# Kernel optimization log

Hardware: AMD Instinct MI355X
Metric: run time of the kernel (lower is better)

## Reference

```python
import jax, jax.numpy as jnp
import numpy as np

DIM = 1024
N_HEAD = 16
SEQ = 2048
GATE_IN = 12
ROPE_BASE = 10000.0
ATTN_SCALE = 0.1
EPS = 1e-6


def setup_inputs() -> dict:
    key = jax.random.key(0)
    ks = jax.random.split(key, 8)
    std = 0.5 * DIM ** -0.5
    bound = (3.0 ** 0.5) * std
    x = jax.random.normal(ks[0], (1, SEQ, DIM), dtype=jnp.float32)
    v1 = jax.random.normal(ks[1], (1, SEQ, DIM), dtype=jnp.float32)
    Wq = jax.random.uniform(ks[2], (DIM, DIM), jnp.float32, -bound, bound)
    Wk = jax.random.uniform(ks[3], (DIM, DIM), jnp.float32, -bound, bound)
    Wv = jax.random.uniform(ks[4], (DIM, DIM), jnp.float32, -bound, bound)
    # original zero-inits c_proj/attn_gate; use small random so output is non-trivial
    Wproj = jax.random.normal(ks[5], (DIM, DIM), dtype=jnp.float32) * 0.02
    Wgate = jax.random.normal(ks[6], (N_HEAD, GATE_IN), dtype=jnp.float32) * 0.02
    lamb = jnp.float32(0.5)
    return {"x": x, "v1": v1, "Wq": Wq, "Wk": Wk, "Wv": Wv,
            "Wproj": Wproj, "lamb": lamb, "Wgate": Wgate}


def _rms_norm(t):
    return t * jax.lax.rsqrt(jnp.mean(jnp.square(t), axis=-1, keepdims=True) + EPS)


def _rotary(t):
    # t: [B, T, H, hd]; rotates halves per the module's sign convention
    B, T, H, hd = t.shape
    d = hd // 2
    inv_freq = 1.0 / (ROPE_BASE ** (jnp.arange(0, hd, 2, dtype=jnp.float32) / hd))  # [d]
    freqs = jnp.arange(T, dtype=jnp.float32)[:, None] * inv_freq[None, :]  # [T, d]
    cos = jnp.cos(freqs)[None, :, None, :]
    sin = jnp.sin(freqs)[None, :, None, :]
    x1, x2 = t[..., :d], t[..., d:]
    y1 = x1 * cos + x2 * sin
    y2 = -x1 * sin + x2 * cos
    return jnp.concatenate([y1, y2], axis=-1)


def reference(x, v1, Wq, Wk, Wv, Wproj, lamb, Wgate):
    B, T, dim = x.shape
    H = Wgate.shape[0]
    hd = dim // H

    q = (x @ Wq.T).reshape(B, T, H, hd)
    k = (x @ Wk.T).reshape(B, T, H, hd)
    v = (x @ Wv.T).reshape(B, T, H, hd)

    # lambda-blended value mixing with residual value stream v1
    v = (1.0 - lamb) * v + lamb * v1.reshape(B, T, H, hd)

    q, k = _rms_norm(q), _rms_norm(k)
    q, k = _rotary(q), _rotary(k)

    # causal attention with fixed scale 0.1 (flex_attention block-sparse causal)
    scores = jnp.einsum("bthd,bshd->bhts", q, k) * ATTN_SCALE  # [B,H,T,T]
    causal = jnp.tril(jnp.ones((T, T), dtype=bool))
    scores = jnp.where(causal[None, None], scores, jnp.float32(-1e30))
    probs = jax.nn.softmax(scores, axis=-1)
    y = jnp.einsum("bhts,bshd->bthd", probs, v)  # [B,T,H,hd]

    # sigmoid gate from the first 12 channels of x, per head
    gate = jax.nn.sigmoid(x[..., :Wgate.shape[1]] @ Wgate.T)[..., None]  # [B,T,H,1]
    y = (y * gate).reshape(B, T, dim)
    y = y @ Wproj.T
    return y, v1
```

## Files before the change

kernel.cpp:

```cpp
#include <hip/hip_runtime.h>
#include <hip/hip_bf16.h>

#define T_SEQ 2048
#define NH 16
#define HD 64
#define SCALE_LOG2E 0.14426950408889634f

typedef __attribute__((ext_vector_type(8))) short bf16x8;
typedef __attribute__((ext_vector_type(4))) short bf16x4;
typedef __attribute__((ext_vector_type(4))) float f32x4;

__device__ __forceinline__ short f2bs(float f) {
  union { float f; unsigned u; } v; v.f = f;
  unsigned r = v.u + 0x7fffu + ((v.u >> 16) & 1u);
  return (short)(r >> 16);
}

__device__ __forceinline__ float bs2f(short s) {
  union { unsigned u; float f; } v;
  v.u = ((unsigned)(unsigned short)s) << 16;
  return v.f;
}

__device__ __forceinline__ unsigned cvt_pk_bf16(float lo, float hi) {
  unsigned r;
  asm("v_cvt_pk_bf16_f32 %0, %1, %2" : "=v"(r) : "v"(lo), "v"(hi));
  return r;
}

__device__ __forceinline__ void gload16(const short* g, short* l) {
  __builtin_amdgcn_global_load_lds(
      (const __attribute__((address_space(1))) void*)g,
      (__attribute__((address_space(3))) void*)l, 16, 0, 0);
}

__global__ __launch_bounds__(256) void cvtT(const float* __restrict__ x,
                                            const float* __restrict__ wq,
                                            const float* __restrict__ wk,
                                            const float* __restrict__ wv,
                                            const float* __restrict__ wp,
                                            short* __restrict__ xbT,
                                            short* __restrict__ wqkvT,
                                            short* __restrict__ wpjT) {
  __shared__ __attribute__((aligned(16))) short lv[64][136];
  const int rt = blockIdx.x;
  const int tid = threadIdx.x;
  const float* src; short* dst; int srow0, drow0, R;
  if (rt < 32)      { src = x;  dst = xbT;   R = 2048; srow0 = rt * 64;        drow0 = srow0; }
  else if (rt < 48) { src = wq; dst = wqkvT; R = 3072; srow0 = (rt - 32) * 64; drow0 = srow0; }
  else if (rt < 64) { src = wk; dst = wqkvT; R = 3072; srow0 = (rt - 48) * 64; drow0 = srow0 + 1024; }
  else if (rt < 80) { src = wv; dst = wqkvT; R = 3072; srow0 = (rt - 64) * 64; drow0 = srow0 + 2048; }
  else              { src = wp; dst = wpjT;  R = 1024; srow0 = (rt - 80) * 64; drow0 = srow0; }
  const int c0 = blockIdx.y * 16;
  #pragma unroll
  for (int it = 0; it < 8; ++it) {
    int e = it * 256 + tid;
    int r = e >> 5, c4 = e & 31;
    float4 v = *(const float4*)&src[(size_t)(srow0 + r) * 1024 + blockIdx.y * 128 + c4 * 4];
    bf16x4 o; o[0] = f2bs(v.x); o[1] = f2bs(v.y); o[2] = f2bs(v.z); o[3] = f2bs(v.w);
    *(bf16x4*)&lv[r][c4 * 4] = o;
  }
  __syncthreads();
  #pragma unroll
  for (int it = 0; it < 4; ++it) {
    int e = it * 256 + tid;
    int kc = e >> 6, r = e & 63;
    bf16x8 w = *(const bf16x8*)&lv[r][kc * 8];
    *(bf16x8*)&dst[((size_t)(c0 + kc) * R + drow0 + r) * 8] = w;
  }
}

__global__ __launch_bounds__(256) void gate_rope(const float* __restrict__ x,
                                                 const float* __restrict__ Wg,
                                                 float* __restrict__ gate,
                                                 float2* __restrict__ rope) {
  int id = blockIdx.x * 256 + threadIdx.x;
  int t = id >> 4, h = id & 15;
  float acc = 0.f;
  #pragma unroll
  for (int i = 0; i < 12; ++i) acc += x[(size_t)t * 1024 + i] * Wg[h * 12 + i];
  gate[id] = 1.f / (1.f + __expf(-acc));
  #pragma unroll
  for (int j = 0; j < 2; ++j) {
    int e = id * 2 + j;
    int tt = e >> 5, p = e & 31;
    float invf = __builtin_exp2f(-0.41524101186092f * (float)p);
    float s, c;
    sincosf((float)tt * invf, &s, &c);
    rope[e] = make_float2(c, s);
  }
}

struct GemmSmem {
  union {
    struct { short As[3][4][128][8]; short Bs[3][4][128][8]; } g;
    short lv[128][130];
  };
};
template <bool QKV>
__global__ __launch_bounds__(256) void gemm128(const short* __restrict__ A,
                                               const short* __restrict__ B,
                                               float* __restrict__ C,
                                               short* __restrict__ qb,
                                               short* __restrict__ kb,
                                               short* __restrict__ vt,
                                               const float* __restrict__ v1,
                                               const float* __restrict__ lambp,
                                               const float2* __restrict__ rope,
                                               int M, int N, int K) {
  __shared__ GemmSmem sm;
  const int tid = threadIdx.x;
  const int lane = tid & 63, wid = tid >> 6;
  const int lr = lane & 15, lg = lane >> 4;
  const int wm = (wid >> 1) * 64, wn = (wid & 1) * 64;
  const int bm = blockIdx.x * 128, bn = blockIdx.y * 128;
  const short* Ap = A + ((size_t)wid * M + bm + lane) * 8;
  const short* Bp = B + ((size_t)wid * N + bn + lane) * 8;
  f32x4 acc[4][4] = {};
  auto stage = [&](int buf, int k0) {
    gload16(Ap + (size_t)k0 * M,       &sm.g.As[buf][wid][0][0]);
    gload16(Ap + (size_t)k0 * M + 512, &sm.g.As[buf][wid][64][0]);
    gload16(Bp + (size_t)k0 * N,       &sm.g.Bs[buf][wid][0][0]);
    gload16(Bp + (size_t)k0 * N + 512, &sm.g.Bs[buf][wid][64][0]);
  };
  auto compute = [&](int buf) {
    bf16x8 af[4], bfr[4];
    #pragma unroll
    for (int m = 0; m < 4; ++m) af[m] = *(const bf16x8*)&sm.g.As[buf][lg][wm + m * 16 + lr][0];
    #pragma unroll
    for (int n = 0; n < 4; ++n) bfr[n] = *(const bf16x8*)&sm.g.Bs[buf][lg][wn + n * 16 + lr][0];
    #pragma unroll
    for (int m = 0; m < 4; ++m)
      #pragma unroll
      for (int n = 0; n < 4; ++n)
        acc[m][n] = __builtin_amdgcn_mfma_f32_16x16x32_bf16(af[m], bfr[n], acc[m][n], 0, 0, 0);
  };
  const int nsteps = K >> 5;
  stage(0, 0);
  stage(1, 32);
  int cur = 0;
  for (int ks = 0; ks < nsteps - 1; ++ks) {
    asm volatile("s_waitcnt vmcnt(4)" ::: "memory");
    __builtin_amdgcn_s_barrier();
    __builtin_amdgcn_sched_barrier(0);
    int s2 = cur + 2; if (s2 >= 3) s2 -= 3;
    if (ks + 2 < nsteps) stage(s2, (ks + 2) * 32);
    compute(cur);
    cur = (cur == 2) ? 0 : cur + 1;
  }
  asm volatile("s_waitcnt vmcnt(0)" ::: "memory");
  __builtin_amdgcn_s_barrier();
  __builtin_amdgcn_sched_barrier(0);
  compute(cur);

  if constexpr (QKV) {
    if (bn < 2048) {
      const bool isq = (bn < 1024);
      short* dst = isq ? qb : kb;
      const int h = ((bn + wn) & 1023) >> 6;
      #pragma unroll
      for (int m = 0; m < 4; ++m)
        #pragma unroll
        for (int r = 0; r < 4; ++r) {
          const int t = bm + wm + m * 16 + 4 * lg + r;
          float ss = acc[m][0][r] * acc[m][0][r] + acc[m][1][r] * acc[m][1][r]
                   + acc[m][2][r] * acc[m][2][r] + acc[m][3][r] * acc[m][3][r];
          ss += __shfl_xor(ss, 1);
          ss += __shfl_xor(ss, 2);
          ss += __shfl_xor(ss, 4);
          ss += __shfl_xor(ss, 8);
          const float rms = rsqrtf(ss * (1.f / 64.f) + 1e-6f);
          short* row = dst + ((size_t)h * T_SEQ + t) * 64;
          #pragma unroll
          for (int n2 = 0; n2 < 2; ++n2) {
            float x1 = acc[m][n2][r] * rms, x2 = acc[m][n2 + 2][r] * rms;
            float2 cs = rope[t * 32 + n2 * 16 + lr];
            float y1 = x1 * cs.x + x2 * cs.y;
            float y2 = x2 * cs.x - x1 * cs.y;
            if (isq) { y1 *= SCALE_LOG2E; y2 *= SCALE_LOG2E; }
            row[n2 * 16 + lr] = f2bs(y1);
            row[32 + n2 * 16 + lr] = f2bs(y2);
          }
        }
    } else {
      const float Lb = *lambp;
      const int h0 = (bn - 2048) >> 6;
      __syncthreads();
      #pragma unroll
      for (int m = 0; m < 4; ++m)
        #pragma unroll
        for (int r = 0; r < 4; ++r) {
          const int tl = wm + m * 16 + 4 * lg + r;
          const size_t vrow = (size_t)(bm + tl) * 1024 + h0 * 64;
          #pragma unroll
          for (int n = 0; n < 4; ++n) {
            const int col = wn + n * 16 + lr;
            float w = v1[vrow + col];
            sm.lv[tl][col] = f2bs((1.f - Lb) * acc[m][n][r] + Lb * w);
          }
        }
      __syncthreads();
      #pragma unroll
      for (int it = 0; it < 8; ++it) {
        int u = it * 256 + tid;
        int c0 = (u & 15) * 8;
        int d = (u >> 4) & 63;
        int hh = u >> 10;
        bf16x8 w;
        #pragma unroll
        for (int j = 0; j < 8; ++j) {
          int c = c0 + j;
          int src = (c & 96) | ((c & 1) << 4) | ((c >> 1) & 15);
          w[j] = sm.lv[src][hh * 64 + d];
        }
        *(bf16x8*)&vt[((size_t)(h0 + hh) * 64 + d) * T_SEQ + bm + c0] = w;
      }
    }
  } else {
    #pragma unroll
    for (int m = 0; m < 4; ++m)
      #pragma unroll
      for (int r = 0; r < 4; ++r) {
        const int t = bm + wm + m * 16 + 4 * lg + r;
        float* Cr = C + (size_t)t * N + bn + wn + lr;
        #pragma unroll
        for (int n = 0; n < 4; ++n) Cr[n * 16] = acc[m][n][r];
      }
  }
}

__global__ __launch_bounds__(256) void attn(const short* __restrict__ qb,
                                            const short* __restrict__ kb,
                                            const short* __restrict__ vtp,
                                            short* __restrict__ partO,
                                            float* __restrict__ partL) {
  __shared__ __attribute__((aligned(16))) short Ks[2][4096];
  __shared__ __attribute__((aligned(16))) short Vs[2][4096];
  __shared__ __attribute__((aligned(16))) short p_lds[4][16][72];
  const int head = blockIdx.x & 15;
  const int b = blockIdx.x >> 4;
  int strip, qg;
  if (b < 32)      { strip = 0; qg = 31 - b; }
  else if (b < 56) { strip = 1; qg = 63 - b; }
  else if (b < 72) { strip = 2; qg = 87 - b; }
  else             { strip = 3; qg = 103 - b; }
  const int nt = min(8, qg + 1 - strip * 8);
  const int lane = threadIdx.x & 63, wid = threadIdx.x >> 6;
  const int lr = lane & 15, lg = lane >> 4;
  const int qt0 = qg * 64 + wid * 16;
  const short* Q = qb + (size_t)head * (T_SEQ * HD);
  const short* Kp = kb + (size_t)head * (T_SEQ * HD);
  const short* Vt = vtp + (size_t)head * (HD * T_SEQ);
  short (*P)[72] = p_lds[wid];

  bf16x8 aq0 = *(const bf16x8*)&Q[(size_t)(qt0 + lr) * HD + 8 * lg];
  bf16x8 aq1 = *(const bf16x8*)&Q[(size_t)(qt0 + lr) * HD + 32 + 8 * lg];
  f32x4 accO[4] = {};
  float lsum[4] = {0.f, 0.f, 0.f, 0.f};

  auto stage = [&](int buf, int jg) {
    const int kv0 = jg * 64;
    #pragma unroll
    for (int i = 0; i < 2; ++i) {
      int s = i * 256 + wid * 64 + lane;
      int row = s >> 3;
      int cG = (s & 7) ^ (row & 7);
      gload16(Kp + (size_t)(kv0 + row) * HD + cG * 8,
              &Ks[buf][(size_t)(i * 256 + wid * 64) * 8]);
      gload16(Vt + (size_t)row * T_SEQ + kv0 + cG * 8,
              &Vs[buf][(size_t)(i * 256 + wid * 64) * 8]);
    }
  };
  stage(0, strip * 8);
  for (int j = 0; j < nt; ++j) {
    const int jg = strip * 8 + j;
    __syncthreads();
    if (j + 1 < nt) stage((j + 1) & 1, jg + 1);
    const short* Kb = Ks[j & 1];
    const short* Vb = Vs[j & 1];
    f32x4 st[4];
    #pragma unroll
    for (int t = 0; t < 4; ++t) {
      int row = 16 * t + lr;
      int c0 = lg ^ (row & 7);
      bf16x8 k0 = *(const bf16x8*)&Kb[row * 64 + c0 * 8];
      bf16x8 k1 = *(const bf16x8*)&Kb[row * 64 + (c0 ^ 4) * 8];
      f32x4 s = {};
      s = __builtin_amdgcn_mfma_f32_16x16x32_bf16(aq0, k0, s, 0, 0, 0);
      s = __builtin_amdgcn_mfma_f32_16x16x32_bf16(aq1, k1, s, 0, 0, 0);
      st[t] = s;
    }
    if (jg == qg) {
      #pragma unroll
      for (int t = 0; t < 4; ++t)
        #pragma unroll
        for (int r = 0; r < 4; ++r)
          st[t][r] = (16 * t + lr > wid * 16 + 4 * lg + r) ? -1e30f : st[t][r];
    }
    #pragma unroll
    for (int r = 0; r < 4; ++r) {
      float p0 = __builtin_exp2f(st[0][r]);
      float p1 = __builtin_exp2f(st[1][r]);
      float p2 = __builtin_exp2f(st[2][r]);
      float p3 = __builtin_exp2f(st[3][r]);
      lsum[r] += (p0 + p1) + (p2 + p3);
      *(unsigned*)&P[4 * lg + r][2 * lr] = cvt_pk_bf16(p0, p1);
      *(unsigned*)&P[4 * lg + r][32 + 2 * lr] = cvt_pk_bf16(p2, p3);
    }
    asm volatile("s_waitcnt lgkmcnt(0)" ::: "memory");
    __builtin_amdgcn_sched_barrier(0);
    bf16x8 pa0 = *(const bf16x8*)&P[lr][8 * lg];
    bf16x8 pa1 = *(const bf16x8*)&P[lr][32 + 8 * lg];
    #pragma unroll
    for (int nv = 0; nv < 4; ++nv) {
      int row0 = nv * 16 + lr;
      int c0 = lg ^ (row0 & 7);
      bf16x8 v0 = *(const bf16x8*)&Vb[row0 * 64 + c0 * 8];
      bf16x8 v1e = *(const bf16x8*)&Vb[row0 * 64 + (c0 ^ 4) * 8];
      accO[nv] = __builtin_amdgcn_mfma_f32_16x16x32_bf16(pa0, v0, accO[nv], 0, 0, 0);
      accO[nv] = __builtin_amdgcn_mfma_f32_16x16x32_bf16(pa1, v1e, accO[nv], 0, 0, 0);
    }
  }
  short* pO = partO + (size_t)(head * 80 + b) * 4096;
  float* pL = partL + (size_t)(head * 80 + b) * 64;
  #pragma unroll
  for (int r = 0; r < 4; ++r) {
    float sres = lsum[r];
    sres += __shfl_xor(sres, 1);
    sres += __shfl_xor(sres, 2);
    sres += __shfl_xor(sres, 4);
    sres += __shfl_xor(sres, 8);
    int row = wid * 16 + 4 * lg + r;
    #pragma unroll
    for (int nv = 0; nv < 4; ++nv)
      pO[row * 64 + nv * 16 + lr] = f2bs(accO[nv][r]);
    if (lr == 0) pL[row] = sres;
  }
}

__global__ __launch_bounds__(256) void attn_reduce(const short* __restrict__ partO,
                                                   const float* __restrict__ partL,
                                                   const float* __restrict__ gate,
                                                   short* __restrict__ obT) {
  const int head = blockIdx.x & 15;
  const int qg = blockIdx.x >> 4;
  const int ns = (qg >> 3) + 1;
  const int tid = threadIdx.x;
  const int row = tid >> 2, q4 = tid & 3;
  const int sbase[4] = {0, 32, 56, 72};
  f32x4 o[4] = {};
  float l = 0.f;
  for (int s = 0; s < ns; ++s) {
    const int slot = head * 80 + sbase[s] + 31 - qg;
    const short* pb = partO + (size_t)slot * 4096;
    #pragma unroll
    for (int c = 0; c < 4; ++c) {
      bf16x4 v = *(const bf16x4*)&pb[row * 64 + q4 * 16 + c * 4];
      #pragma unroll
      for (int j = 0; j < 4; ++j) o[c][j] += bs2f(v[j]);
    }
    l += partL[(size_t)slot * 64 + row];
  }
  const int t = qg * 64 + row;
  const float gs = gate[t * 16 + head] / l;
  const int cg0 = head * 8 + q4 * 2;
  bf16x8 w0, w1;
  #pragma unroll
  for (int j = 0; j < 4; ++j) {
    w0[j]     = f2bs(o[0][j] * gs);
    w0[4 + j] = f2bs(o[1][j] * gs);
    w1[j]     = f2bs(o[2][j] * gs);
    w1[4 + j] = f2bs(o[3][j] * gs);
  }
  *(bf16x8*)&obT[((size_t)cg0 * 2048 + t) * 8] = w0;
  *(bf16x8*)&obT[((size_t)(cg0 + 1) * 2048 + t) * 8] = w1;
}

extern "C" void kernel_launch(void* const* d_in, const int* in_sizes, int n_in,
                              void* d_out, int out_size, void* d_ws, size_t ws_size,
                              hipStream_t stream) {
  const float* x     = (const float*)d_in[0];
  const float* v1    = (const float*)d_in[1];
  const float* Wq    = (const float*)d_in[2];
  const float* Wk    = (const float*)d_in[3];
  const float* Wv    = (const float*)d_in[4];
  const float* Wproj = (const float*)d_in[5];
  const float* lamb  = (const float*)d_in[6];
  const float* Wgate = (const float*)d_in[7];
  float* out = (float*)d_out;

  char* ws = (char*)d_ws;
  short*  xbT   = (short*)(ws);
  short*  wqkvT = (short*)(ws + ((size_t)4  << 20));
  short*  wpjT  = (short*)(ws + ((size_t)10 << 20));
  short*  partO = (short*)(ws + ((size_t)12 << 20));
  float*  partL = (float*)(ws + ((size_t)23 << 20));
  float2* rope  = (float2*)(ws + ((size_t)34 << 20));
  short*  qb    = (short*)(ws + ((size_t)36 << 20));
  short*  kb    = (short*)(ws + ((size_t)40 << 20));
  short*  vt    = (short*)(ws + ((size_t)44 << 20));
  float*  gate  = (float*)(ws + ((size_t)48 << 20));
  short*  obT   = xbT;

  cvtT<<<dim3(96, 8), 256, 0, stream>>>(x, Wq, Wk, Wv, Wproj, xbT, wqkvT, wpjT);
  gate_rope<<<(T_SEQ * NH) / 256, 256, 0, stream>>>(x, Wgate, gate, rope);
  gemm128<true><<<dim3(16, 24), 256, 0, stream>>>(xbT, wqkvT, nullptr, qb, kb, vt,
                                                  v1, lamb, rope, 2048, 3072, 1024);
  attn<<<1280, 256, 0, stream>>>(qb, kb, vt, partO, partL);
  attn_reduce<<<512, 256, 0, stream>>>(partO, partL, gate, obT);
  gemm128<false><<<dim3(16, 8), 256, 0, stream>>>(obT, wpjT, out, nullptr, nullptr,
                                                  nullptr, nullptr, nullptr, nullptr,
                                                  2048, 1024, 1024);
  hipMemcpyAsync(out + (size_t)T_SEQ * 1024, v1,
                 (size_t)T_SEQ * 1024 * sizeof(float),
                 hipMemcpyDeviceToDevice, stream);
}
```

Measured before the change: 79.89 us.

## Fuse prep kernels, drop split-KV attention reduce, and retile projection GEMM

Merges the conversion, gate/rope computation and the v1 output copy into one prep launch. Attention no longer splits the key range into strips, so it no longer writes partial outputs for a separate reduce kernel. Each block now walks the full causal range and applies the normalization and gate directly. The output projection GEMM uses 64-row tiles to launch more blocks. This cuts launches and partial-buffer traffic, but the long causal rows now run serially in one block, which costs parallelism and balance across the 512 attention blocks.

```diff
diff --git a/kernel.cpp b/kernel.cpp
--- a/kernel.cpp
+++ b/kernel.cpp
@@ -16,12 +16,6 @@
   return (short)(r >> 16);
 }
 
-__device__ __forceinline__ float bs2f(short s) {
-  union { unsigned u; float f; } v;
-  v.u = ((unsigned)(unsigned short)s) << 16;
-  return v.f;
-}
-
 __device__ __forceinline__ unsigned cvt_pk_bf16(float lo, float hi) {
   unsigned r;
   asm("v_cvt_pk_bf16_f32 %0, %1, %2" : "=v"(r) : "v"(lo), "v"(hi));
@@ -34,17 +28,52 @@
       (__attribute__((address_space(3))) void*)l, 16, 0, 0);
 }
 
-__global__ __launch_bounds__(256) void cvtT(const float* __restrict__ x,
+__global__ __launch_bounds__(256) void prep(const float* __restrict__ x,
                                             const float* __restrict__ wq,
                                             const float* __restrict__ wk,
                                             const float* __restrict__ wv,
                                             const float* __restrict__ wp,
+                                            const float* __restrict__ v1,
+                                            const float* __restrict__ Wg,
                                             short* __restrict__ xbT,
                                             short* __restrict__ wqkvT,
-                                            short* __restrict__ wpjT) {
-  __shared__ __attribute__((aligned(16))) short lv[64][136];
+                                            short* __restrict__ wpjT,
+                                            float* __restrict__ out2,
+                                            float* __restrict__ gate,
+                                            float2* __restrict__ rope) {
   const int rt = blockIdx.x;
   const int tid = threadIdx.x;
+  if (blockIdx.y == 8) {
+    int id = rt * 256 + tid;
+    int t = id >> 4, h = id & 15;
+    float acc = 0.f;
+    #pragma unroll
+    for (int i = 0; i < 12; ++i) acc += x[(size_t)t * 1024 + i] * Wg[h * 12 + i];
+    gate[id] = 1.f / (1.f + __expf(-acc));
+    #pragma unroll
+    for (int j = 0; j < 2; ++j) {
+      int e = id * 2 + j;
+      int tt = e >> 5, p = e & 31;
+      float invf = __builtin_exp2f(-0.41524101186092f * (float)p);
+      float s, c;
+      sincosf((float)tt * invf, &s, &c);
+      rope[e] = make_float2(c, s);
+    }
+    return;
+  }
+  if (rt >= 96) {
+    const int r0 = (rt - 96) * 64;
+    const float* s = v1 + (size_t)r0 * 1024 + blockIdx.y * 128;
+    float* d = out2 + (size_t)r0 * 1024 + blockIdx.y * 128;
+    #pragma unroll
+    for (int it = 0; it < 8; ++it) {
+      int e = it * 256 + tid;
+      int r = e >> 5, c4 = e & 31;
+      *(float4*)&d[(size_t)r * 1024 + c4 * 4] = *(const float4*)&s[(size_t)r * 1024 + c4 * 4];
+    }
+    return;
+  }
+  __shared__ __attribute__((aligned(16))) short lv[64][136];
   const float* src; short* dst; int srow0, drow0, R;
   if (rt < 32)      { src = x;  dst = xbT;   R = 2048; srow0 = rt * 64;        drow0 = srow0; }
   else if (rt < 48) { src = wq; dst = wqkvT; R = 3072; srow0 = (rt - 32) * 64; drow0 = srow0; }
@@ -70,67 +99,46 @@
   }
 }
 
-__global__ __launch_bounds__(256) void gate_rope(const float* __restrict__ x,
-                                                 const float* __restrict__ Wg,
-                                                 float* __restrict__ gate,
-                                                 float2* __restrict__ rope) {
-  int id = blockIdx.x * 256 + threadIdx.x;
-  int t = id >> 4, h = id & 15;
-  float acc = 0.f;
-  #pragma unroll
-  for (int i = 0; i < 12; ++i) acc += x[(size_t)t * 1024 + i] * Wg[h * 12 + i];
-  gate[id] = 1.f / (1.f + __expf(-acc));
-  #pragma unroll
-  for (int j = 0; j < 2; ++j) {
-    int e = id * 2 + j;
-    int tt = e >> 5, p = e & 31;
-    float invf = __builtin_exp2f(-0.41524101186092f * (float)p);
-    float s, c;
-    sincosf((float)tt * invf, &s, &c);
-    rope[e] = make_float2(c, s);
-  }
-}
-
-struct GemmSmem {
-  union {
-    struct { short As[3][4][128][8]; short Bs[3][4][128][8]; } g;
+template <int BM, bool QKV>
+__global__ __launch_bounds__(256) void gemm(const short* __restrict__ A,
+                                            const short* __restrict__ B,
+                                            float* __restrict__ C,
+                                            short* __restrict__ qb,
+                                            short* __restrict__ kb,
+                                            short* __restrict__ vt,
+                                            const float* __restrict__ v1,
+                                            const float* __restrict__ lambp,
+                                            const float2* __restrict__ rope,
+                                            int M, int N, int K) {
+  constexpr int MF = BM / 32;
+  constexpr int LA = BM / 64;
+  __shared__ union {
+    struct { short As[3][4][BM][8]; short Bs[3][4][128][8]; } g;
     short lv[128][130];
-  };
-};
-template <bool QKV>
-__global__ __launch_bounds__(256) void gemm128(const short* __restrict__ A,
-                                               const short* __restrict__ B,
-                                               float* __restrict__ C,
-                                               short* __restrict__ qb,
-                                               short* __restrict__ kb,
-                                               short* __restrict__ vt,
-                                               const float* __restrict__ v1,
-                                               const float* __restrict__ lambp,
-                                               const float2* __restrict__ rope,
-                                               int M, int N, int K) {
-  __shared__ GemmSmem sm;
+  } sm;
   const int tid = threadIdx.x;
   const int lane = tid & 63, wid = tid >> 6;
   const int lr = lane & 15, lg = lane >> 4;
-  const int wm = (wid >> 1) * 64, wn = (wid & 1) * 64;
-  const int bm = blockIdx.x * 128, bn = blockIdx.y * 128;
+  const int wm = (wid >> 1) * (BM / 2), wn = (wid & 1) * 64;
+  const int bm = blockIdx.x * BM, bn = blockIdx.y * 128;
   const short* Ap = A + ((size_t)wid * M + bm + lane) * 8;
   const short* Bp = B + ((size_t)wid * N + bn + lane) * 8;
-  f32x4 acc[4][4] = {};
+  f32x4 acc[MF][4] = {};
   auto stage = [&](int buf, int k0) {
-    gload16(Ap + (size_t)k0 * M,       &sm.g.As[buf][wid][0][0]);
-    gload16(Ap + (size_t)k0 * M + 512, &sm.g.As[buf][wid][64][0]);
+    #pragma unroll
+    for (int g = 0; g < LA; ++g)
+      gload16(Ap + (size_t)k0 * M + g * 512, &sm.g.As[buf][wid][64 * g][0]);
     gload16(Bp + (size_t)k0 * N,       &sm.g.Bs[buf][wid][0][0]);
     gload16(Bp + (size_t)k0 * N + 512, &sm.g.Bs[buf][wid][64][0]);
   };
   auto compute = [&](int buf) {
-    bf16x8 af[4], bfr[4];
-    #pragma unroll
-    for (int m = 0; m < 4; ++m) af[m] = *(const bf16x8*)&sm.g.As[buf][lg][wm + m * 16 + lr][0];
+    bf16x8 af[MF], bfr[4];
+    #pragma unroll
+    for (int m = 0; m < MF; ++m) af[m] = *(const bf16x8*)&sm.g.As[buf][lg][wm + m * 16 + lr][0];
     #pragma unroll
     for (int n = 0; n < 4; ++n) bfr[n] = *(const bf16x8*)&sm.g.Bs[buf][lg][wn + n * 16 + lr][0];
     #pragma unroll
-    for (int m = 0; m < 4; ++m)
+    for (int m = 0; m < MF; ++m)
       #pragma unroll
       for (int n = 0; n < 4; ++n)
         acc[m][n] = __builtin_amdgcn_mfma_f32_16x16x32_bf16(af[m], bfr[n], acc[m][n], 0, 0, 0);
@@ -140,7 +148,8 @@
   stage(1, 32);
   int cur = 0;
   for (int ks = 0; ks < nsteps - 1; ++ks) {
-    asm volatile("s_waitcnt vmcnt(4)" ::: "memory");
+    if constexpr (BM == 128) asm volatile("s_waitcnt vmcnt(4)" ::: "memory");
+    else                     asm volatile("s_waitcnt vmcnt(3)" ::: "memory");
     __builtin_amdgcn_s_barrier();
     __builtin_amdgcn_sched_barrier(0);
     int s2 = cur + 2; if (s2 >= 3) s2 -= 3;
@@ -159,7 +168,7 @@
       short* dst = isq ? qb : kb;
       const int h = ((bn + wn) & 1023) >> 6;
       #pragma unroll
-      for (int m = 0; m < 4; ++m)
+      for (int m = 0; m < MF; ++m)
         #pragma unroll
         for (int r = 0; r < 4; ++r) {
           const int t = bm + wm + m * 16 + 4 * lg + r;
@@ -187,7 +196,7 @@
       const int h0 = (bn - 2048) >> 6;
       __syncthreads();
       #pragma unroll
-      for (int m = 0; m < 4; ++m)
+      for (int m = 0; m < MF; ++m)
         #pragma unroll
         for (int r = 0; r < 4; ++r) {
           const int tl = wm + m * 16 + 4 * lg + r;
@@ -218,7 +227,7 @@
     }
   } else {
     #pragma unroll
-    for (int m = 0; m < 4; ++m)
+    for (int m = 0; m < MF; ++m)
       #pragma unroll
       for (int r = 0; r < 4; ++r) {
         const int t = bm + wm + m * 16 + 4 * lg + r;
@@ -232,19 +241,14 @@
 __global__ __launch_bounds__(256) void attn(const short* __restrict__ qb,
                                             const short* __restrict__ kb,
                                             const short* __restrict__ vtp,
-                                            short* __restrict__ partO,
-                                            float* __restrict__ partL) {
+                                            const float* __restrict__ gate,
+                                            short* __restrict__ obT) {
   __shared__ __attribute__((aligned(16))) short Ks[2][4096];
   __shared__ __attribute__((aligned(16))) short Vs[2][4096];
   __shared__ __attribute__((aligned(16))) short p_lds[4][16][72];
   const int head = blockIdx.x & 15;
-  const int b = blockIdx.x >> 4;
-  int strip, qg;
-  if (b < 32)      { strip = 0; qg = 31 - b; }
-  else if (b < 56) { strip = 1; qg = 63 - b; }
-  else if (b < 72) { strip = 2; qg = 87 - b; }
-  else             { strip = 3; qg = 103 - b; }
-  const int nt = min(8, qg + 1 - strip * 8);
+  const int qg = 31 - (blockIdx.x >> 4);
+  const int nt = qg + 1;
   const int lane = threadIdx.x & 63, wid = threadIdx.x >> 6;
   const int lr = lane & 15, lg = lane >> 4;
   const int qt0 = qg * 64 + wid * 16;
@@ -271,11 +275,10 @@
               &Vs[buf][(size_t)(i * 256 + wid * 64) * 8]);
     }
   };
-  stage(0, strip * 8);
+  stage(0, 0);
   for (int j = 0; j < nt; ++j) {
-    const int jg = strip * 8 + j;
     __syncthreads();
-    if (j + 1 < nt) stage((j + 1) & 1, jg + 1);
+    if (j + 1 < nt) stage((j + 1) & 1, j + 1);
     const short* Kb = Ks[j & 1];
     const short* Vb = Vs[j & 1];
     f32x4 st[4];
@@ -290,7 +293,7 @@
       s = __builtin_amdgcn_mfma_f32_16x16x32_bf16(aq1, k1, s, 0, 0, 0);
       st[t] = s;
     }
-    if (jg == qg) {
+    if (j == qg) {
       #pragma unroll
       for (int t = 0; t < 4; ++t)
         #pragma unroll
@@ -321,8 +324,6 @@
       accO[nv] = __builtin_amdgcn_mfma_f32_16x16x32_bf16(pa1, v1e, accO[nv], 0, 0, 0);
     }
   }
-  short* pO = partO + (size_t)(head * 80 + b) * 4096;
-  float* pL = partL + (size_t)(head * 80 + b) * 64;
   #pragma unroll
   for (int r = 0; r < 4; ++r) {
     float sres = lsum[r];
@@ -330,50 +331,15 @@
     sres += __shfl_xor(sres, 2);
     sres += __shfl_xor(sres, 4);
     sres += __shfl_xor(sres, 8);
-    int row = wid * 16 + 4 * lg + r;
-    #pragma unroll
-    for (int nv = 0; nv < 4; ++nv)
-      pO[row * 64 + nv * 16 + lr] = f2bs(accO[nv][r]);
-    if (lr == 0) pL[row] = sres;
-  }
-}
-
-__global__ __launch_bounds__(256) void attn_reduce(const short* __restrict__ partO,
-                                                   const float* __restrict__ partL,
-                                                   const float* __restrict__ gate,
-                                                   short* __restrict__ obT) {
-  const int head = blockIdx.x & 15;
-  const int qg = blockIdx.x >> 4;
-  const int ns = (qg >> 3) + 1;
-  const int tid = threadIdx.x;
-  const int row = tid >> 2, q4 = tid & 3;
-  const int sbase[4] = {0, 32, 56, 72};
-  f32x4 o[4] = {};
-  float l = 0.f;
-  for (int s = 0; s < ns; ++s) {
-    const int slot = head * 80 + sbase[s] + 31 - qg;
-    const short* pb = partO + (size_t)slot * 4096;
-    #pragma unroll
-    for (int c = 0; c < 4; ++c) {
-      bf16x4 v = *(const bf16x4*)&pb[row * 64 + q4 * 16 + c * 4];
-      #pragma unroll
-      for (int j = 0; j < 4; ++j) o[c][j] += bs2f(v[j]);
-    }
-    l += partL[(size_t)slot * 64 + row];
-  }
-  const int t = qg * 64 + row;
-  const float gs = gate[t * 16 + head] / l;
-  const int cg0 = head * 8 + q4 * 2;
-  bf16x8 w0, w1;
-  #pragma unroll
-  for (int j = 0; j < 4; ++j) {
-    w0[j]     = f2bs(o[0][j] * gs);
-    w0[4 + j] = f2bs(o[1][j] * gs);
-    w1[j]     = f2bs(o[2][j] * gs);
-    w1[4 + j] = f2bs(o[3][j] * gs);
-  }
-  *(bf16x8*)&obT[((size_t)cg0 * 2048 + t) * 8] = w0;
-  *(bf16x8*)&obT[((size_t)(cg0 + 1) * 2048 + t) * 8] = w1;
+    const int t = qt0 + 4 * lg + r;
+    const float gs = gate[t * 16 + head] / sres;
+    #pragma unroll
+    for (int nv = 0; nv < 4; ++nv) {
+      const int col = nv * 16 + lr;
+      obT[((size_t)(head * 8 + (col >> 3)) * T_SEQ + t) * 8 + (col & 7)] =
+          f2bs(accO[nv][r] * gs);
+    }
+  }
 }
 
 extern "C" void kernel_launch(void* const* d_in, const int* in_sizes, int n_in,
@@ -393,8 +359,6 @@
   short*  xbT   = (short*)(ws);
   short*  wqkvT = (short*)(ws + ((size_t)4  << 20));
   short*  wpjT  = (short*)(ws + ((size_t)10 << 20));
-  short*  partO = (short*)(ws + ((size_t)12 << 20));
-  float*  partL = (float*)(ws + ((size_t)23 << 20));
   float2* rope  = (float2*)(ws + ((size_t)34 << 20));
   short*  qb    = (short*)(ws + ((size_t)36 << 20));
   short*  kb    = (short*)(ws + ((size_t)40 << 20));
@@ -402,16 +366,13 @@
   float*  gate  = (float*)(ws + ((size_t)48 << 20));
   short*  obT   = xbT;
 
-  cvtT<<<dim3(96, 8), 256, 0, stream>>>(x, Wq, Wk, Wv, Wproj, xbT, wqkvT, wpjT);
-  gate_rope<<<(T_SEQ * NH) / 256, 256, 0, stream>>>(x, Wgate, gate, rope);
-  gemm128<true><<<dim3(16, 24), 256, 0, stream>>>(xbT, wqkvT, nullptr, qb, kb, vt,
-                                                  v1, lamb, rope, 2048, 3072, 1024);
-  attn<<<1280, 256, 0, stream>>>(qb, kb, vt, partO, partL);
-  attn_reduce<<<512, 256, 0, stream>>>(partO, partL, gate, obT);
-  gemm128<false><<<dim3(16, 8), 256, 0, stream>>>(obT, wpjT, out, nullptr, nullptr,
-                                                  nullptr, nullptr, nullptr, nullptr,
-                                                  2048, 1024, 1024);
-  hipMemcpyAsync(out + (size_t)T_SEQ * 1024, v1,
-                 (size_t)T_SEQ * 1024 * sizeof(float),
-                 hipMemcpyDeviceToDevice, stream);
-}
+  prep<<<dim3(128, 9), 256, 0, stream>>>(x, Wq, Wk, Wv, Wproj, v1, Wgate,
+                                         xbT, wqkvT, wpjT,
+                                         out + (size_t)T_SEQ * 1024, gate, rope);
+  gemm<128, true><<<dim3(16, 24), 256, 0, stream>>>(xbT, wqkvT, nullptr, qb, kb, vt,
+                                                    v1, lamb, rope, 2048, 3072, 1024);
+  attn<<<512, 256, 0, stream>>>(qb, kb, vt, gate, obT);
+  gemm<64, false><<<dim3(32, 8), 256, 0, stream>>>(obT, wpjT, out, nullptr, nullptr,
+                                                   nullptr, nullptr, nullptr, nullptr,
+                                                   2048, 1024, 1024);
+}
```

Result: slower. 82.97 us (+3.9%).
